# Performance work log

Measured on AMD Instinct MI355X. Metric: run time of the kernel, lower is better.

Reference implementation:

```python
import jax, jax.numpy as jnp
import numpy as np

B, S, H, E, K, DFF = 4, 2048, 1024, 8, 2, 4096


def setup_inputs() -> dict:
    key = jax.random.key(0)
    k0, k1, k2, k3 = jax.random.split(key, 4)
    sc = 0.02
    return {
        "x": jax.random.normal(k0, (B, S, H), jnp.float32),
        "gate_W": jax.random.normal(k1, (H, E), jnp.float32) * sc,
        "gate_b": jnp.zeros((E,), jnp.float32),
        "W1": jax.random.normal(k2, (H, DFF), jnp.float32) * sc,
        "b1": jnp.zeros((DFF,), jnp.float32),
        "W2": jax.random.normal(k3, (DFF, H), jnp.float32) * sc,
        "b2": jnp.zeros((H,), jnp.float32),
    }


def reference(x, gate_W, gate_b, W1, b1, W2, b2):
    b, s, h = x.shape
    x_flat = x.reshape(-1, h)                      # [T, H]
    gate_scores = x_flat @ gate_W + gate_b         # [T, E]
    top_k_scores, top_k_idx = jax.lax.top_k(gate_scores, K)   # [T, K]
    top_k_w = jax.nn.softmax(top_k_scores, axis=-1)           # [T, K]

    # All experts share the same weights (ModuleList reuses one module), so
    # sum_i w_i * expert_i(x) == expert(x) * sum_i w_i. top_k indices are
    # unique per token, so the per-token combine weight is sum of top-k weights.
    hdd = jax.nn.gelu(x_flat @ W1 + b1, approximate=False)    # [T, DFF]
    y = hdd @ W2 + b2                                         # [T, H]
    tok_w = top_k_w.sum(axis=-1)                              # [T] (== 1.0)
    output = (y * tok_w[:, None]).reshape(b, s, h)

    expert_load = gate_scores.mean(axis=0)                    # [E]
    aux_loss = (expert_load ** 2).sum()
    exp_counts = jnp.zeros((E,), jnp.int32).at[top_k_idx.ravel()].add(1)
    return output, aux_loss, exp_counts
```

## Files before the change

### kernel.cpp

```cpp
#include <hip/hip_runtime.h>
#include <hip/hip_bf16.h>
#include <math.h>

#define Tn   8192
#define Hn   1024
#define En   8
#define DFFn 4096

typedef __attribute__((ext_vector_type(8))) short bf16x8;
typedef __attribute__((ext_vector_type(4))) float f32x4;

static __device__ inline unsigned short f2bf(float f) {
    __hip_bfloat16 h = __float2bfloat16(f);
    return __builtin_bit_cast(unsigned short, h);
}

__global__ __launch_bounds__(256) void prep(
    const float* __restrict__ W1, unsigned short* __restrict__ W1t,
    const float* __restrict__ x, const float* __restrict__ gW,
    const float* __restrict__ gb, unsigned short* __restrict__ xbf,
    float* __restrict__ tokw, float* __restrict__ load_sum,
    int* __restrict__ counts)
{
    __shared__ float smem[8 * 1024 + En];
    __shared__ int   s_cnt[En];
    const int tid = threadIdx.x;
    const int id  = blockIdx.x;

    if (id >= 1024) {
        const int tb = id - 1024;
        float* tile = smem;
        const int bx = tb & 127, by = tb >> 7;
        const int n0 = bx * 32, k0 = by * 32;
        const int r  = tid >> 3, c4 = (tid & 7) * 4;
        float4 v = *(const float4*)(W1 + (size_t)(k0 + r) * DFFn + n0 + c4);
        tile[(c4 + 0) * 33 + r] = v.x;
        tile[(c4 + 1) * 33 + r] = v.y;
        tile[(c4 + 2) * 33 + r] = v.z;
        tile[(c4 + 3) * 33 + r] = v.w;
        __syncthreads();
        ushort4 pk;
        pk.x = f2bf(tile[r * 33 + c4 + 0]);
        pk.y = f2bf(tile[r * 33 + c4 + 1]);
        pk.z = f2bf(tile[r * 33 + c4 + 2]);
        pk.w = f2bf(tile[r * 33 + c4 + 3]);
        *(ushort4*)(W1t + (size_t)(n0 + r) * Hn + k0 + c4) = pk;
        return;
    }

    float* gwt    = smem;
    float* s_load = smem + 8 * 1024;
    if (tid < En) { s_load[tid] = 0.f; s_cnt[tid] = 0; }
    #pragma unroll
    for (int i = 0; i < 32; ++i) {
        int f = tid + i * 256;
        gwt[(f & 7) * 1024 + (f >> 3)] = gW[f];
    }
    __syncthreads();

    const int lane = tid & 63;
    const int wv   = tid >> 6;

    for (int tok = id * 4 + wv; tok < Tn; tok += 4096) {
        const float4* xr = (const float4*)(x + (size_t)tok * Hn);
        float acc[8] = {0.f,0.f,0.f,0.f,0.f,0.f,0.f,0.f};
        #pragma unroll
        for (int j = 0; j < Hn / 256; ++j) {
            int h4 = j * 64 + lane;
            float4 xv = xr[h4];
            ushort4 pk;
            pk.x = f2bf(xv.x); pk.y = f2bf(xv.y);
            pk.z = f2bf(xv.z); pk.w = f2bf(xv.w);
            ((ushort4*)xbf)[(size_t)tok * (Hn / 4) + h4] = pk;
            #pragma unroll
            for (int e = 0; e < 8; ++e) {
                const float4 w = *(const float4*)(gwt + e * 1024 + h4 * 4);
                acc[e] += xv.x * w.x + xv.y * w.y + xv.z * w.z + xv.w * w.w;
            }
        }
        #pragma unroll
        for (int e = 0; e < 8; ++e) {
            float v = acc[e];
            #pragma unroll
            for (int off = 32; off > 0; off >>= 1) v += __shfl_xor(v, off, 64);
            acc[e] = v + gb[e];
        }
        if (lane == 0) {
            #pragma unroll
            for (int e = 0; e < 8; ++e) atomicAdd(&s_load[e], acc[e]);
            int i1 = 0; float v1 = acc[0];
            #pragma unroll
            for (int e = 1; e < 8; ++e) if (acc[e] > v1) { v1 = acc[e]; i1 = e; }
            int i2 = -1; float v2 = -3.0e38f;
            #pragma unroll
            for (int e = 0; e < 8; ++e) if (e != i1 && acc[e] > v2) { v2 = acc[e]; i2 = e; }
            atomicAdd(&s_cnt[i1], 1);
            atomicAdd(&s_cnt[i2], 1);
            float e2 = __expf(v2 - v1);
            float t  = 1.0f + e2;
            tokw[tok] = 1.0f / t + e2 / t;
        }
    }
    __syncthreads();
    if (tid < En) {
        atomicAdd(&load_sum[tid], s_load[tid]);
        atomicAdd(&counts[tid],   s_cnt[tid]);
    }
}

template<int EPI>
__global__ __launch_bounds__(256) void gemm_bt(
    const __hip_bfloat16* __restrict__ A,
    const __hip_bfloat16* __restrict__ Bt,
    const float* __restrict__ bias,
    const float* __restrict__ tokw,
    void* __restrict__ C, int N, int K, int nxlog2, int nblk,
    const float* __restrict__ W2, unsigned short* __restrict__ W2t,
    const float* __restrict__ load_sum, const int* __restrict__ counts,
    float* __restrict__ out_tail)
{
    __shared__ __hip_bfloat16 sA[128 * 64];
    __shared__ __hip_bfloat16 sB[128 * 64];

    const int tid = threadIdx.x;
    const int id  = blockIdx.x;

    if (EPI == 0 && id >= nblk) {
        const int tb = id - nblk;
        float* tile = (float*)sA;
        const int bx = tb & 31, by = tb >> 5;
        const int n0 = bx * 32, k0 = by * 32;
        const int r  = tid >> 3, c4 = (tid & 7) * 4;
        float4 v = *(const float4*)(W2 + (size_t)(k0 + r) * Hn + n0 + c4);
        tile[(c4 + 0) * 33 + r] = v.x;
        tile[(c4 + 1) * 33 + r] = v.y;
        tile[(c4 + 2) * 33 + r] = v.z;
        tile[(c4 + 3) * 33 + r] = v.w;
        __syncthreads();
        ushort4 pk;
        pk.x = f2bf(tile[r * 33 + c4 + 0]);
        pk.y = f2bf(tile[r * 33 + c4 + 1]);
        pk.z = f2bf(tile[r * 33 + c4 + 2]);
        pk.w = f2bf(tile[r * 33 + c4 + 3]);
        *(ushort4*)(W2t + (size_t)(n0 + r) * DFFn + k0 + c4) = pk;
        if (tb == 0 && tid == 0) {
            float aux = 0.f;
            #pragma unroll
            for (int e = 0; e < En; ++e) {
                float m = load_sum[e] * (1.0f / (float)Tn);
                aux += m * m;
            }
            out_tail[0] = aux;
            #pragma unroll
            for (int e = 0; e < En; ++e) out_tail[1 + e] = (float)counts[e];
        }
        return;
    }

    const int lane = tid & 63;
    const int wv   = tid >> 6;
    const int wm   = (wv >> 1) * 64;
    const int wn   = (wv & 1) * 64;

    const int xcd    = id & 7;
    const int slot_  = id >> 3;
    const int bx     = slot_ & ((1 << nxlog2) - 1);
    const int ylocal = slot_ >> nxlog2;
    const int y_per  = (nblk >> 3) >> nxlog2;
    const int by     = xcd * y_per + ylocal;

    const int m0 = by * 128, n0 = bx * 128;

    f32x4 acc[4][4];
    const f32x4 zero = {0.f, 0.f, 0.f, 0.f};
    #pragma unroll
    for (int i = 0; i < 4; ++i)
        #pragma unroll
        for (int j = 0; j < 4; ++j) acc[i][j] = zero;

    const int wq   = tid >> 6;
    const int slot = tid & 7;
    const __hip_bfloat16* gAj[4];
    const __hip_bfloat16* gBj[4];
    int loff[4];
    #pragma unroll
    for (int j = 0; j < 4; ++j) {
        const int row = wq * 32 + j * 8 + ((tid & 63) >> 3);
        const int c   = (slot - (row >> 1)) & 7;
        gAj[j]  = A  + (size_t)(m0 + row) * K + c * 8;
        gBj[j]  = Bt + (size_t)(n0 + row) * K + c * 8;
        loff[j] = row * 64 + slot * 8;
    }

    const int fr = lane & 15;
    const int fq = lane >> 4;

    for (int k0 = 0; k0 < K; k0 += 64) {
        __syncthreads();
        #pragma unroll
        for (int j = 0; j < 4; ++j) {
            __builtin_amdgcn_global_load_lds(
                (const __attribute__((address_space(1))) void*)(gAj[j] + k0),
                (__attribute__((address_space(3))) void*)(sA + loff[j]), 16, 0, 0);
            __builtin_amdgcn_global_load_lds(
                (const __attribute__((address_space(1))) void*)(gBj[j] + k0),
                (__attribute__((address_space(3))) void*)(sB + loff[j]), 16, 0, 0);
        }
        __syncthreads();

        #pragma unroll
        for (int ks = 0; ks < 2; ++ks) {
            bf16x8 af[4], bfr[4];
            #pragma unroll
            for (int mi = 0; mi < 4; ++mi) {
                const int r = wm + mi * 16 + fr;
                const int s = (ks * 4 + fq + ((r >> 1) & 7)) & 7;
                af[mi] = *(const bf16x8*)(sA + r * 64 + s * 8);
            }
            #pragma unroll
            for (int ni = 0; ni < 4; ++ni) {
                const int r = wn + ni * 16 + fr;
                const int s = (ks * 4 + fq + ((r >> 1) & 7)) & 7;
                bfr[ni] = *(const bf16x8*)(sB + r * 64 + s * 8);
            }
            #pragma unroll
            for (int mi = 0; mi < 4; ++mi)
                #pragma unroll
                for (int ni = 0; ni < 4; ++ni)
                    acc[mi][ni] = __builtin_amdgcn_mfma_f32_16x16x32_bf16(
                        af[mi], bfr[ni], acc[mi][ni], 0, 0, 0);
        }
    }

    #pragma unroll
    for (int mi = 0; mi < 4; ++mi) {
        #pragma unroll
        for (int ni = 0; ni < 4; ++ni) {
            const int col   = n0 + wn + ni * 16 + (lane & 15);
            const int rbase = m0 + wm + mi * 16 + (lane >> 4) * 4;
            const float bv  = bias[col];
            #pragma unroll
            for (int i = 0; i < 4; ++i) {
                const int row = rbase + i;
                float v = acc[mi][ni][i] + bv;
                if (EPI == 0) {
                    float vv = v * v;
                    float z  = v * __fmaf_rn(vv, -0.07135607f, -1.59576912f);
                    float e  = __expf(z);
                    float g  = v * __builtin_amdgcn_rcpf(1.0f + e);
                    ((__hip_bfloat16*)C)[(size_t)row * N + col] = __float2bfloat16(g);
                } else {
                    ((float*)C)[(size_t)row * N + col] = v * tokw[row];
                }
            }
        }
    }
}

extern "C" void kernel_launch(void* const* d_in, const int* in_sizes, int n_in,
                              void* d_out, int out_size, void* d_ws, size_t ws_size,
                              hipStream_t stream)
{
    const float* x  = (const float*)d_in[0];
    const float* gW = (const float*)d_in[1];
    const float* gb = (const float*)d_in[2];
    const float* W1 = (const float*)d_in[3];
    const float* b1 = (const float*)d_in[4];
    const float* W2 = (const float*)d_in[5];
    const float* b2 = (const float*)d_in[6];
    float* out = (float*)d_out;

    char* ws = (char*)d_ws;
    __hip_bfloat16* xbf = (__hip_bfloat16*)ws;  ws += (size_t)Tn * Hn * 2;
    __hip_bfloat16* W1t = (__hip_bfloat16*)ws;  ws += (size_t)Hn * DFFn * 2;
    __hip_bfloat16* W2t = (__hip_bfloat16*)ws;  ws += (size_t)Hn * DFFn * 2;
    __hip_bfloat16* hdd = (__hip_bfloat16*)ws;  ws += (size_t)Tn * DFFn * 2;
    float* tokw     = (float*)ws;               ws += (size_t)Tn * 4;
    float* load_sum = (float*)ws;               ws += En * 4;
    int*   counts   = (int*)ws;                 ws += En * 4;

    hipMemsetAsync(load_sum, 0, En * 4 * 2, stream);

    prep<<<5120, 256, 0, stream>>>(W1, (unsigned short*)W1t, x, gW, gb,
                                   (unsigned short*)xbf, tokw, load_sum, counts);

    gemm_bt<0><<<2048 + 4096, 256, 0, stream>>>(
        xbf, W1t, b1, nullptr, hdd, DFFn, Hn, 5, 2048,
        W2, (unsigned short*)W2t, load_sum, counts, out + (size_t)Tn * Hn);
    gemm_bt<1><<<512, 256, 0, stream>>>(
        hdd, W2t, b2, tokw, out, Hn, DFFn, 3, 512,
        nullptr, nullptr, nullptr, nullptr, nullptr);
}
```

Baseline: 313.9 us.

## Rewrite GEMMs as 8-wave 256-row tiles with double-buffered LDS pipelining

Replaces the 128x128 single-buffered GEMM with a templated 512-thread kernel that uses 256xBN tiles, double-buffered dynamic LDS, and an interleaved schedule. That schedule issues global-to-LDS loads for upcoming k-tiles between MFMA quarter-blocks, using explicit waitcnt, barriers and setprio. It is meant to hide memory latency and raise MFMA utilisation. The W2 transpose moves from the first GEMM launch into the prep kernel, so the GEMM grid contains only compute tiles plus one tail block for aux/counts. The cost is higher register and LDS pressure, and a fragile hand-tuned synchronisation scheme.

```diff
diff --git a/kernel.cpp b/kernel.cpp
--- a/kernel.cpp
+++ b/kernel.cpp
@@ -17,6 +17,7 @@
 
 __global__ __launch_bounds__(256) void prep(
     const float* __restrict__ W1, unsigned short* __restrict__ W1t,
+    const float* __restrict__ W2, unsigned short* __restrict__ W2t,
     const float* __restrict__ x, const float* __restrict__ gW,
     const float* __restrict__ gb, unsigned short* __restrict__ xbf,
     float* __restrict__ tokw, float* __restrict__ load_sum,
@@ -26,6 +27,27 @@
     __shared__ int   s_cnt[En];
     const int tid = threadIdx.x;
     const int id  = blockIdx.x;
+
+    if (id >= 5120) {
+        const int tb = id - 5120;
+        float* tile = smem;
+        const int bx = tb & 31, by = tb >> 5;
+        const int n0 = bx * 32, k0 = by * 32;
+        const int r  = tid >> 3, c4 = (tid & 7) * 4;
+        float4 v = *(const float4*)(W2 + (size_t)(k0 + r) * Hn + n0 + c4);
+        tile[(c4 + 0) * 33 + r] = v.x;
+        tile[(c4 + 1) * 33 + r] = v.y;
+        tile[(c4 + 2) * 33 + r] = v.z;
+        tile[(c4 + 3) * 33 + r] = v.w;
+        __syncthreads();
+        ushort4 pk;
+        pk.x = f2bf(tile[r * 33 + c4 + 0]);
+        pk.y = f2bf(tile[r * 33 + c4 + 1]);
+        pk.z = f2bf(tile[r * 33 + c4 + 2]);
+        pk.w = f2bf(tile[r * 33 + c4 + 3]);
+        *(ushort4*)(W2t + (size_t)(n0 + r) * DFFn + k0 + c4) = pk;
+        return;
+    }
 
     if (id >= 1024) {
         const int tb = id - 1024;
@@ -108,42 +130,37 @@
     }
 }
 
-template<int EPI>
-__global__ __launch_bounds__(256) void gemm_bt(
+
+static __device__ inline bf16x8 ldsfrag(const char* base, int row, int chunk) {
+    return *(const bf16x8*)(base + row * 128 + (((chunk) ^ (row & 7)) << 4));
+}
+
+template<int BN, int WM, int WN, int EPI>
+__global__ __launch_bounds__(512, 2) void gemm8(
     const __hip_bfloat16* __restrict__ A,
     const __hip_bfloat16* __restrict__ Bt,
     const float* __restrict__ bias,
     const float* __restrict__ tokw,
-    void* __restrict__ C, int N, int K, int nxlog2, int nblk,
-    const float* __restrict__ W2, unsigned short* __restrict__ W2t,
+    void* __restrict__ C, int N, int K, int nx,
     const float* __restrict__ load_sum, const int* __restrict__ counts,
-    float* __restrict__ out_tail)
+    float* __restrict__ out_tail, int nblk)
 {
-    __shared__ __hip_bfloat16 sA[128 * 64];
-    __shared__ __hip_bfloat16 sB[128 * 64];
+    constexpr int BM = 256;
+    constexpr int MR = (BM / WM) / 16;
+    constexpr int NR = (BN / WN) / 16;
+    constexpr int AU = BM / 64;
+    constexpr int BU = BN / 64;
+    constexpr int ABYTES = BM * 64 * 2;
+    constexpr int BBYTES = BN * 64 * 2;
+    constexpr int TILEB  = ABYTES + BBYTES;
+
+    extern __shared__ char lds[];
 
     const int tid = threadIdx.x;
     const int id  = blockIdx.x;
 
     if (EPI == 0 && id >= nblk) {
-        const int tb = id - nblk;
-        float* tile = (float*)sA;
-        const int bx = tb & 31, by = tb >> 5;
-        const int n0 = bx * 32, k0 = by * 32;
-        const int r  = tid >> 3, c4 = (tid & 7) * 4;
-        float4 v = *(const float4*)(W2 + (size_t)(k0 + r) * Hn + n0 + c4);
-        tile[(c4 + 0) * 33 + r] = v.x;
-        tile[(c4 + 1) * 33 + r] = v.y;
-        tile[(c4 + 2) * 33 + r] = v.z;
-        tile[(c4 + 3) * 33 + r] = v.w;
-        __syncthreads();
-        ushort4 pk;
-        pk.x = f2bf(tile[r * 33 + c4 + 0]);
-        pk.y = f2bf(tile[r * 33 + c4 + 1]);
-        pk.z = f2bf(tile[r * 33 + c4 + 2]);
-        pk.w = f2bf(tile[r * 33 + c4 + 3]);
-        *(ushort4*)(W2t + (size_t)(n0 + r) * DFFn + k0 + c4) = pk;
-        if (tb == 0 && tid == 0) {
+        if (tid == 0) {
             float aux = 0.f;
             #pragma unroll
             for (int e = 0; e < En; ++e) {
@@ -157,93 +174,150 @@
         return;
     }
 
+    int wg = id;
+    { int xcd = wg & 7, idx = wg >> 3; wg = xcd * (nblk >> 3) + idx; }
+    const int by = wg / nx, bx = wg % nx;
+    const int m0 = by * BM, n0 = bx * BN;
+
     const int lane = tid & 63;
-    const int wv   = tid >> 6;
-    const int wm   = (wv >> 1) * 64;
-    const int wn   = (wv & 1) * 64;
-
-    const int xcd    = id & 7;
-    const int slot_  = id >> 3;
-    const int bx     = slot_ & ((1 << nxlog2) - 1);
-    const int ylocal = slot_ >> nxlog2;
-    const int y_per  = (nblk >> 3) >> nxlog2;
-    const int by     = xcd * y_per + ylocal;
-
-    const int m0 = by * 128, n0 = bx * 128;
-
-    f32x4 acc[4][4];
+    const int wid  = tid >> 6;
+    const int wn   = wid % WN;
+    const int wm   = wid / WN;
+    const int wrow = wm * (BM / WM);
+    const int wcol = wn * (BN / WN);
+    const int fr   = lane & 15;
+    const int fq   = lane >> 4;
+
+    const int sr = tid >> 3;
+    const int sc = (tid & 7) ^ (sr & 7);
+    unsigned aOff[AU], bOff[BU];
+    #pragma unroll
+    for (int u = 0; u < AU; ++u)
+        aOff[u] = (unsigned)((m0 + u * 64 + sr) * K + sc * 8);
+    #pragma unroll
+    for (int u = 0; u < BU; ++u)
+        bOff[u] = (unsigned)((n0 + u * 64 + sr) * K + sc * 8);
+
+#define STA(b, u, kt) __builtin_amdgcn_global_load_lds( \
+    (const __attribute__((address_space(1))) void*)(A + aOff[u] + (unsigned)(kt) * 64u), \
+    (__attribute__((address_space(3))) void*)(lds + (b) * TILEB + (u) * 8192 + tid * 16), 16, 0, 0)
+#define STB(b, u, kt) __builtin_amdgcn_global_load_lds( \
+    (const __attribute__((address_space(1))) void*)(Bt + bOff[u] + (unsigned)(kt) * 64u), \
+    (__attribute__((address_space(3))) void*)(lds + (b) * TILEB + ABYTES + (u) * 8192 + tid * 16), 16, 0, 0)
+
+    bf16x8 af[MR / 2][2];
+    bf16x8 bfr[4][2];
+    f32x4  acc[MR][NR];
     const f32x4 zero = {0.f, 0.f, 0.f, 0.f};
     #pragma unroll
-    for (int i = 0; i < 4; ++i)
+    for (int i = 0; i < MR; ++i)
         #pragma unroll
-        for (int j = 0; j < 4; ++j) acc[i][j] = zero;
-
-    const int wq   = tid >> 6;
-    const int slot = tid & 7;
-    const __hip_bfloat16* gAj[4];
-    const __hip_bfloat16* gBj[4];
-    int loff[4];
-    #pragma unroll
-    for (int j = 0; j < 4; ++j) {
-        const int row = wq * 32 + j * 8 + ((tid & 63) >> 3);
-        const int c   = (slot - (row >> 1)) & 7;
-        gAj[j]  = A  + (size_t)(m0 + row) * K + c * 8;
-        gBj[j]  = Bt + (size_t)(n0 + row) * K + c * 8;
-        loff[j] = row * 64 + slot * 8;
-    }
-
-    const int fr = lane & 15;
-    const int fq = lane >> 4;
-
-    for (int k0 = 0; k0 < K; k0 += 64) {
-        __syncthreads();
+        for (int j = 0; j < NR; ++j) acc[i][j] = zero;
+
+#define RDA(b, half) do { _Pragma("unroll") \
+    for (int m_ = 0; m_ < MR / 2; ++m_) { _Pragma("unroll") \
+        for (int ks_ = 0; ks_ < 2; ++ks_) \
+            af[m_][ks_] = ldsfrag(lds + (b) * TILEB, \
+                wrow + ((half) * (MR / 2) + m_) * 16 + fr, ks_ * 4 + fq); } } while (0)
+
+#define RDB(b, half) do { _Pragma("unroll") \
+    for (int n_ = 0; n_ < 2; ++n_) { _Pragma("unroll") \
+        for (int ks_ = 0; ks_ < 2; ++ks_) \
+            bfr[(half) * 2 + n_][ks_] = ldsfrag(lds + (b) * TILEB + ABYTES, \
+                wcol + ((half) * 2 + n_) * 16 + fr, ks_ * 4 + fq); } } while (0)
+
+#define MFMAQ(hm, hn) do { \
+    __builtin_amdgcn_s_setprio(1); \
+    _Pragma("unroll") \
+    for (int m_ = 0; m_ < MR / 2; ++m_) { _Pragma("unroll") \
+        for (int n_ = 0; n_ < 2; ++n_) { _Pragma("unroll") \
+            for (int ks_ = 0; ks_ < 2; ++ks_) \
+                acc[(hm) * (MR / 2) + m_][(hn) * 2 + n_] = \
+                    __builtin_amdgcn_mfma_f32_16x16x32_bf16( \
+                        af[m_][ks_], bfr[(hn) * 2 + n_][ks_], \
+                        acc[(hm) * (MR / 2) + m_][(hn) * 2 + n_], 0, 0, 0); } } \
+    __builtin_amdgcn_s_setprio(0); } while (0)
+
+#define MIDSYNC do { \
+    __builtin_amdgcn_sched_barrier(0); \
+    __builtin_amdgcn_s_barrier(); \
+    asm volatile("s_waitcnt lgkmcnt(0)" ::: "memory"); \
+    __builtin_amdgcn_sched_barrier(0); } while (0)
+
+#define ENDBAR do { \
+    __builtin_amdgcn_sched_barrier(0); \
+    __builtin_amdgcn_s_barrier(); \
+    __builtin_amdgcn_sched_barrier(0); } while (0)
+
+#define DRAIN do { \
+    if constexpr (WM == 2) asm volatile("s_waitcnt vmcnt(6)" ::: "memory"); \
+    else                   asm volatile("s_waitcnt vmcnt(4)" ::: "memory"); \
+    __builtin_amdgcn_sched_barrier(0); } while (0)
+
+    const int KT = K >> 6;
+
+    if constexpr (WM == 2) {
+        STA(0,0,0); STA(0,1,0); STA(0,2,0); STA(0,3,0);
+        STB(0,0,0); STB(0,1,0); STB(0,2,0); STB(0,3,0);
+        STA(1,0,1); STA(1,2,1);
+        STB(1,0,1); STB(1,1,1); STB(1,2,1); STB(1,3,1);
+        asm volatile("s_waitcnt vmcnt(6)" ::: "memory");
+    } else {
+        STA(0,0,0); STA(0,1,0); STA(0,2,0); STA(0,3,0);
+        STB(0,0,0); STB(0,1,0);
+        STA(1,0,1); STA(1,1,1);
+        STB(1,0,1); STB(1,1,1);
+        asm volatile("s_waitcnt vmcnt(4)" ::: "memory");
+    }
+    __builtin_amdgcn_sched_barrier(0);
+    __builtin_amdgcn_s_barrier();
+    __builtin_amdgcn_sched_barrier(0);
+
+    for (int i = 0; i < (KT >> 1); ++i) {
+        const int t1 = 2 * i + 1;
+        const int c2 = (2 * i + 2 < KT) ? 2 * i + 2 : KT - 1;
+        const int c3 = (2 * i + 3 < KT) ? 2 * i + 3 : KT - 1;
+
+        RDA(0, 0); RDB(0, 0);
+        if constexpr (WM == 2) { STA(1,1,t1); STA(1,3,t1); }
+        else                   { STA(1,2,t1); STA(1,3,t1); }
+        MIDSYNC; MFMAQ(0, 0); ENDBAR;
+        RDB(0, 1);
+        if constexpr (WM == 2) { STA(0,0,c2); STA(0,2,c2); }
+        MIDSYNC; MFMAQ(0, 1); ENDBAR;
+        RDA(0, 1);
+        STB(0,0,c2); STB(0,1,c2);
+        MIDSYNC; MFMAQ(1, 0); ENDBAR;
+        if constexpr (WM == 2) { STB(0,2,c2); STB(0,3,c2); }
+        else                   { STA(0,0,c2); STA(0,1,c2); }
+        MIDSYNC; MFMAQ(1, 1); DRAIN; ENDBAR;
+        RDA(1, 0); RDB(1, 0);
+        if constexpr (WM == 2) { STA(0,1,c2); STA(0,3,c2); }
+        else                   { STA(0,2,c2); STA(0,3,c2); }
+        MIDSYNC; MFMAQ(0, 0); ENDBAR;
+        RDB(1, 1);
+        if constexpr (WM == 2) { STA(1,0,c3); STA(1,2,c3); }
+        MIDSYNC; MFMAQ(0, 1); ENDBAR;
+        RDA(1, 1);
+        STB(1,0,c3); STB(1,1,c3);
+        MIDSYNC; MFMAQ(1, 0); ENDBAR;
+        if constexpr (WM == 2) { STB(1,2,c3); STB(1,3,c3); }
+        else                   { STA(1,0,c3); STA(1,1,c3); }
+        MIDSYNC; MFMAQ(1, 1); DRAIN; ENDBAR;
+    }
+
+    #pragma unroll
+    for (int mi = 0; mi < MR; ++mi) {
         #pragma unroll
-        for (int j = 0; j < 4; ++j) {
-            __builtin_amdgcn_global_load_lds(
-                (const __attribute__((address_space(1))) void*)(gAj[j] + k0),
-                (__attribute__((address_space(3))) void*)(sA + loff[j]), 16, 0, 0);
-            __builtin_amdgcn_global_load_lds(
-                (const __attribute__((address_space(1))) void*)(gBj[j] + k0),
-                (__attribute__((address_space(3))) void*)(sB + loff[j]), 16, 0, 0);
-        }
-        __syncthreads();
-
-        #pragma unroll
-        for (int ks = 0; ks < 2; ++ks) {
-            bf16x8 af[4], bfr[4];
-            #pragma unroll
-            for (int mi = 0; mi < 4; ++mi) {
-                const int r = wm + mi * 16 + fr;
-                const int s = (ks * 4 + fq + ((r >> 1) & 7)) & 7;
-                af[mi] = *(const bf16x8*)(sA + r * 64 + s * 8);
-            }
-            #pragma unroll
-            for (int ni = 0; ni < 4; ++ni) {
-                const int r = wn + ni * 16 + fr;
-                const int s = (ks * 4 + fq + ((r >> 1) & 7)) & 7;
-                bfr[ni] = *(const bf16x8*)(sB + r * 64 + s * 8);
-            }
-            #pragma unroll
-            for (int mi = 0; mi < 4; ++mi)
-                #pragma unroll
-                for (int ni = 0; ni < 4; ++ni)
-                    acc[mi][ni] = __builtin_amdgcn_mfma_f32_16x16x32_bf16(
-                        af[mi], bfr[ni], acc[mi][ni], 0, 0, 0);
-        }
-    }
-
-    #pragma unroll
-    for (int mi = 0; mi < 4; ++mi) {
-        #pragma unroll
-        for (int ni = 0; ni < 4; ++ni) {
-            const int col   = n0 + wn + ni * 16 + (lane & 15);
-            const int rbase = m0 + wm + mi * 16 + (lane >> 4) * 4;
+        for (int ni = 0; ni < NR; ++ni) {
+            const int col   = n0 + wcol + ni * 16 + (lane & 15);
+            const int rbase = m0 + wrow + mi * 16 + (lane >> 4) * 4;
             const float bv  = bias[col];
             #pragma unroll
-            for (int i = 0; i < 4; ++i) {
-                const int row = rbase + i;
-                float v = acc[mi][ni][i] + bv;
-                if (EPI == 0) {
+            for (int i2 = 0; i2 < 4; ++i2) {
+                const int row = rbase + i2;
+                float v = acc[mi][ni][i2] + bv;
+                if constexpr (EPI == 0) {
                     float vv = v * v;
                     float z  = v * __fmaf_rn(vv, -0.07135607f, -1.59576912f);
                     float e  = __expf(z);
@@ -255,6 +329,15 @@
             }
         }
     }
+
+#undef STA
+#undef STB
+#undef RDA
+#undef RDB
+#undef MFMAQ
+#undef MIDSYNC
+#undef ENDBAR
+#undef DRAIN
 }
 
 extern "C" void kernel_launch(void* const* d_in, const int* in_sizes, int n_in,
@@ -279,15 +362,29 @@
     float* load_sum = (float*)ws;               ws += En * 4;
     int*   counts   = (int*)ws;                 ws += En * 4;
 
+    static bool attr_done = false;
+    if (!attr_done) {
+        (void)hipFuncSetAttribute(
+            reinterpret_cast<const void*>(&gemm8<256, 2, 4, 0>),
+            hipFuncAttributeMaxDynamicSharedMemorySize, 131072);
+        (void)hipFuncSetAttribute(
+            reinterpret_cast<const void*>(&gemm8<128, 4, 2, 1>),
+            hipFuncAttributeMaxDynamicSharedMemorySize, 98304);
+        attr_done = true;
+    }
+
     hipMemsetAsync(load_sum, 0, En * 4 * 2, stream);
 
-    prep<<<5120, 256, 0, stream>>>(W1, (unsigned short*)W1t, x, gW, gb,
-                                   (unsigned short*)xbf, tokw, load_sum, counts);
-
-    gemm_bt<0><<<2048 + 4096, 256, 0, stream>>>(
-        xbf, W1t, b1, nullptr, hdd, DFFn, Hn, 5, 2048,
-        W2, (unsigned short*)W2t, load_sum, counts, out + (size_t)Tn * Hn);
-    gemm_bt<1><<<512, 256, 0, stream>>>(
-        hdd, W2t, b2, tokw, out, Hn, DFFn, 3, 512,
-        nullptr, nullptr, nullptr, nullptr, nullptr);
-}
+    prep<<<9216, 256, 0, stream>>>(W1, (unsigned short*)W1t,
+                                   W2, (unsigned short*)W2t,
+                                   x, gW, gb, (unsigned short*)xbf,
+                                   tokw, load_sum, counts);
+
+    gemm8<256, 2, 4, 0><<<513, 512, 131072, stream>>>(
+        xbf, W1t, b1, nullptr, hdd, DFFn, Hn, 16,
+        load_sum, counts, out + (size_t)Tn * Hn, 512);
+
+    gemm8<128, 4, 2, 1><<<256, 512, 98304, stream>>>(
+        hdd, W2t, b2, tokw, out, Hn, DFFn, 8,
+        nullptr, nullptr, nullptr, 256);
+}
```

Result: faster. 270.1 us (-13.9%).
